# Optimization experiments

Hardware: AMD Instinct MI355X
Metric: run time of the kernel (lower is better)

The kernel has to match this reference:

```python
import jax, jax.numpy as jnp
import numpy as np

E = 8          # num_experts
TOP_K = 2      # router top-k
ALPHA = 1.702  # swigluoai alpha
LIMIT = 7.0    # swigluoai clamp limit


def setup_inputs() -> dict:
    key = jax.random.key(0)
    ks = jax.random.split(key, 7)
    B, S, H, I = 2, 1024, 1024, 1024
    s = 1.0 / np.sqrt(H)  # keep activations O(1), realistic init scale
    return {
        "x": jax.random.normal(ks[0], (B, S, H), jnp.float32),
        "router_weight": jax.random.normal(ks[1], (E, H), jnp.float32) * s,
        "router_bias": jax.random.normal(ks[2], (E,), jnp.float32) * 0.01,
        "w1": jax.random.normal(ks[3], (E, H, 2 * I), jnp.float32) * s,  # interleaved gate/up
        "w1_bias": jax.random.normal(ks[4], (E, 2 * I), jnp.float32) * 0.01,
        "w2": jax.random.normal(ks[5], (E, I, H), jnp.float32) * s,
        "w2_bias": jax.random.normal(ks[6], (E, H), jnp.float32) * 0.01,
    }


def _moe(x, router_weight, router_bias, w1, w1_bias, w2, w2_bias):
    B, S, H = x.shape
    xf = x.reshape(-1, H)                                   # [T, H]
    # ---- router: softmax over expert logits, then top-k ----
    logits = xf @ router_weight.T + router_bias             # [T, E]
    probs = jax.nn.softmax(logits, axis=-1)
    expert_weights, expert_ids = jax.lax.top_k(probs, TOP_K)  # [T, k]
    # combine weights scattered to dense [T, E] (no normalization: normalize_expert_weights=None)
    combine = jnp.sum(jax.nn.one_hot(expert_ids, E, dtype=xf.dtype)
                      * expert_weights[..., None], axis=1)  # [T, E]
    # ---- grouped MLP, expressed densely per expert (reference semantics) ----
    h = jnp.einsum('th,ehi->eti', xf, w1) + w1_bias[:, None, :]   # [E, T, 2I]
    gate = h[..., 0::2]                                          # interleaved layout
    up = h[..., 1::2]
    gate = jnp.minimum(gate, LIMIT)                              # swigluoai: clamp gate max
    up = jnp.clip(up, -LIMIT, LIMIT)                             # clamp up both sides
    glu = gate * jax.nn.sigmoid(gate * ALPHA)
    act = (up + 1.0) * glu                                       # [E, T, I]
    y = jnp.einsum('eti,eih->eth', act, w2) + w2_bias[:, None, :]  # [E, T, H]
    out = jnp.einsum('eth,te->th', y, combine)                   # weighted combine
    return out.reshape(B, S, H), expert_weights


def reference(x, router_weight, router_bias, w1, w1_bias, w2, w2_bias):
    return _moe(x, router_weight, router_bias, w1, w1_bias, w2, w2_bias)
```

## Files before the change

kernel.cpp:

```cpp
#include <hip/hip_runtime.h>
#include <cstdint>
#include <cstddef>

typedef unsigned short u16;
typedef unsigned int u32;
typedef short bf16x8 __attribute__((ext_vector_type(8)));
typedef float floatx4 __attribute__((ext_vector_type(4)));

#define GLD16(gp, sp) __builtin_amdgcn_global_load_lds(                      \
    (const __attribute__((address_space(1))) void*)(gp),                     \
    (__attribute__((address_space(3))) void*)(sp), 16, 0, 0)

__device__ __forceinline__ u16 f2bf(float f) {
  unsigned u = __float_as_uint(f);
  u += 0x7fffu + ((u >> 16) & 1u);
  return (u16)(u >> 16);
}

__global__ __launch_bounds__(256) void prep_kernel(
    const float* __restrict__ x, const float* __restrict__ rw, const float* __restrict__ rbias,
    u16* __restrict__ xb, float* __restrict__ ew,
    int* __restrict__ row_token, float* __restrict__ row_scale, int* __restrict__ cnt) {
  const int b = blockIdx.x, tid = threadIdx.x;
  if (b < 1024) {
    const float4* in4 = (const float4*)x;
    ushort4* out4 = (ushort4*)xb;
    int i = (b << 8) + tid;
#pragma unroll
    for (int rep = 0; rep < 2; ++rep, i += 262144) {
      float4 v = in4[i];
      ushort4 o;
      o.x = f2bf(v.x); o.y = f2bf(v.y); o.z = f2bf(v.z); o.w = f2bf(v.w);
      out4[i] = o;
    }
  } else {
    const int wave = tid >> 6, lane = tid & 63;
    const int t = ((b - 1024) << 2) + wave;
    const float4* xv = (const float4*)(x + (size_t)t * 1024);
    float acc[8];
#pragma unroll
    for (int e = 0; e < 8; ++e) acc[e] = 0.f;
    for (int j = lane; j < 256; j += 64) {
      float4 xx = xv[j];
#pragma unroll
      for (int e = 0; e < 8; ++e) {
        float4 wv = ((const float4*)(rw + (size_t)e * 1024))[j];
        acc[e] += xx.x * wv.x + xx.y * wv.y + xx.z * wv.z + xx.w * wv.w;
      }
    }
#pragma unroll
    for (int e = 0; e < 8; ++e) {
      float v = acc[e];
#pragma unroll
      for (int off = 32; off > 0; off >>= 1) v += __shfl_down(v, off);
      acc[e] = v;
    }
    if (lane == 0) {
      float p[8];
      float mx = -1e30f;
#pragma unroll
      for (int e = 0; e < 8; ++e) { p[e] = acc[e] + rbias[e]; mx = fmaxf(mx, p[e]); }
      float sum = 0.f;
#pragma unroll
      for (int e = 0; e < 8; ++e) { p[e] = __expf(p[e] - mx); sum += p[e]; }
      float inv = 1.f / sum;
#pragma unroll
      for (int e = 0; e < 8; ++e) p[e] *= inv;
      int i0 = 0;
#pragma unroll
      for (int e = 1; e < 8; ++e) if (p[e] > p[i0]) i0 = e;
      int i1 = (i0 == 0) ? 1 : 0;
#pragma unroll
      for (int e = 0; e < 8; ++e) if (e != i0 && e != i1 && p[e] > p[i1]) i1 = e;
      ew[t * 2 + 0] = p[i0];
      ew[t * 2 + 1] = p[i1];
      int s0 = atomicAdd(&cnt[i0], 1);
      row_token[(i0 << 11) + s0] = t;
      row_scale[(i0 << 11) + s0] = p[i0];
      int s1 = atomicAdd(&cnt[i1], 1);
      row_token[(i1 << 11) + s1] = t;
      row_scale[(i1 << 11) + s1] = p[i1];
    }
  }
}

__device__ __forceinline__ void stage_bt(const float* __restrict__ src0, int C, int idx,
                                         u16* __restrict__ Bs) {
  const int n = idx & 127, q = idx >> 7;
  const float* src = src0 + (size_t)(q * 8) * C + n;
  float f[8];
#pragma unroll
  for (int j = 0; j < 8; ++j) f[j] = src[(size_t)j * C];
  u32 pk[4];
#pragma unroll
  for (int m = 0; m < 4; ++m) pk[m] = (u32)f2bf(f[2 * m]) | ((u32)f2bf(f[2 * m + 1]) << 16);
  *(uint4*)(Bs + ((n >> 4) << 9) + (q << 7) + ((n & 15) << 3)) =
      make_uint4(pk[0], pk[1], pk[2], pk[3]);
}

__global__ __launch_bounds__(256) void gemm1_act_kernel(
    const u16* __restrict__ xb, const float* __restrict__ w1,
    const float* __restrict__ w1b,
    const int* __restrict__ row_token, const float* __restrict__ row_scale,
    const int* __restrict__ cnt, u16* __restrict__ actS) {
  const int d = blockIdx.x;
  const int xcd = d & 7, j = d >> 3;
  const int colHi = j & 1, rb = (j >> 1) & 15, e = j >> 5;
  if (rb * 128 >= cnt[e]) return;
  const int colBase = (xcd + (colHi << 3)) << 7;
  const int slotB = (e << 11) + (rb << 7);
  __shared__ __align__(16) u16 As[4096];
  __shared__ __align__(16) u16 Bs[4096];
  const int tid = threadIdx.x, lane = tid & 63, wave = tid >> 6;
  const int row16 = lane & 15, chunk = lane >> 4;
  const float* w1e = w1 + (size_t)e * 2097152 + colBase;
  int tk0 = row_token[slotB + wave * 16 + row16];       if (tk0 < 0) tk0 = 0;
  int tk1 = row_token[slotB + (wave + 4) * 16 + row16]; if (tk1 < 0) tk1 = 0;
  const u16* aP0 = xb + (size_t)tk0 * 1024 + chunk * 8;
  const u16* aP1 = xb + (size_t)tk1 * 1024 + chunk * 8;
  const int wr = wave >> 1, wc = wave & 1;
  floatx4 acc[4][4];
#pragma unroll
  for (int mi = 0; mi < 4; ++mi)
#pragma unroll
    for (int ni = 0; ni < 4; ++ni) acc[mi][ni] = floatx4{0.f, 0.f, 0.f, 0.f};

  for (int kt = 0; kt < 32; ++kt) {
    const int k = kt * 32;
    GLD16(aP0 + k, As + wave * 512);
    GLD16(aP1 + k, As + (wave + 4) * 512);
    stage_bt(w1e + (size_t)k * 2048, 2048, tid, Bs);
    stage_bt(w1e + (size_t)k * 2048, 2048, tid + 256, Bs);
    __syncthreads();
    bf16x8 af[4], bfr[4];
#pragma unroll
    for (int mi = 0; mi < 4; ++mi) af[mi] = *(const bf16x8*)(As + (wr * 4 + mi) * 512 + lane * 8);
#pragma unroll
    for (int ni = 0; ni < 4; ++ni) bfr[ni] = *(const bf16x8*)(Bs + (wc * 4 + ni) * 512 + lane * 8);
#pragma unroll
    for (int mi = 0; mi < 4; ++mi)
#pragma unroll
      for (int ni = 0; ni < 4; ++ni)
        acc[mi][ni] = __builtin_amdgcn_mfma_f32_16x16x32_bf16(af[mi], bfr[ni], acc[mi][ni], 0, 0, 0);
    __syncthreads();
  }

  const int cl = lane & 15, ql = lane >> 4;
#pragma unroll
  for (int mi = 0; mi < 4; ++mi) {
#pragma unroll
    for (int r = 0; r < 4; ++r) {
      const int slot = slotB + wr * 64 + mi * 16 + ql * 4 + r;
      const float c = row_scale[slot];
#pragma unroll
      for (int ni = 0; ni < 4; ++ni) {
        const int n = colBase + wc * 64 + ni * 16 + cl;
        float v = acc[mi][ni][r] + w1b[e * 2048 + n];
        float o = __shfl_xor(v, 1);
        if ((lane & 1) == 0) {
          float g = fminf(v, 7.f);
          float u = fminf(fmaxf(o, -7.f), 7.f);
          float sg = 1.f / (1.f + __expf(-1.702f * g));
          float a = (u + 1.f) * (g * sg);
          actS[(size_t)slot * 1024 + (n >> 1)] = f2bf(c * a);
        }
      }
    }
  }
}

__global__ __launch_bounds__(256) void gemm2_add_kernel(
    const u16* __restrict__ actS, const float* __restrict__ w2, const float* __restrict__ w2b,
    const int* __restrict__ row_token, const float* __restrict__ row_scale,
    const int* __restrict__ cnt, float* __restrict__ out) {
  const int d = blockIdx.x;
  const int xcd = d & 7, j = d >> 3;
  const int ks = j & 1, rb = (j >> 1) & 15, e = j >> 5;
  if (rb * 128 >= cnt[e]) return;
  const int colBase = xcd << 7;
  const int slotB = (e << 11) + (rb << 7);
  const int k0 = ks << 9;
  __shared__ __align__(16) u16 As[4096];
  __shared__ __align__(16) u16 Bs[4096];
  const int tid = threadIdx.x, lane = tid & 63, wave = tid >> 6;
  const int row16 = lane & 15, chunk = lane >> 4;
  const float* w2e = w2 + (size_t)e * 1048576 + (size_t)k0 * 1024 + colBase;
  const u16* aP0 = actS + (size_t)(slotB + wave * 16 + row16) * 1024 + k0 + chunk * 8;
  const u16* aP1 = actS + (size_t)(slotB + (wave + 4) * 16 + row16) * 1024 + k0 + chunk * 8;
  const int wr = wave >> 1, wc = wave & 1;
  floatx4 acc[4][4];
#pragma unroll
  for (int mi = 0; mi < 4; ++mi)
#pragma unroll
    for (int ni = 0; ni < 4; ++ni) acc[mi][ni] = floatx4{0.f, 0.f, 0.f, 0.f};

  for (int kt = 0; kt < 16; ++kt) {
    const int k = kt * 32;
    GLD16(aP0 + k, As + wave * 512);
    GLD16(aP1 + k, As + (wave + 4) * 512);
    stage_bt(w2e + (size_t)k * 1024, 1024, tid, Bs);
    stage_bt(w2e + (size_t)k * 1024, 1024, tid + 256, Bs);
    __syncthreads();
    bf16x8 af[4], bfr[4];
#pragma unroll
    for (int mi = 0; mi < 4; ++mi) af[mi] = *(const bf16x8*)(As + (wr * 4 + mi) * 512 + lane * 8);
#pragma unroll
    for (int ni = 0; ni < 4; ++ni) bfr[ni] = *(const bf16x8*)(Bs + (wc * 4 + ni) * 512 + lane * 8);
#pragma unroll
    for (int mi = 0; mi < 4; ++mi)
#pragma unroll
      for (int ni = 0; ni < 4; ++ni)
        acc[mi][ni] = __builtin_amdgcn_mfma_f32_16x16x32_bf16(af[mi], bfr[ni], acc[mi][ni], 0, 0, 0);
    __syncthreads();
  }

  const int cl = lane & 15, ql = lane >> 4;
#pragma unroll
  for (int mi = 0; mi < 4; ++mi)
#pragma unroll
    for (int r = 0; r < 4; ++r) {
      const int slot = slotB + wr * 64 + mi * 16 + ql * 4 + r;
      const int tok = row_token[slot];
      if (tok < 0) continue;
      const float p = row_scale[slot];
#pragma unroll
      for (int ni = 0; ni < 4; ++ni) {
        const int col = colBase + wc * 64 + ni * 16 + cl;
        float v = acc[mi][ni][r];
        if (ks == 0) v += p * w2b[e * 1024 + col];
        atomicAdd(out + (size_t)tok * 1024 + col, v);
      }
    }
}

extern "C" void kernel_launch(void* const* d_in, const int* in_sizes, int n_in,
                              void* d_out, int out_size, void* d_ws, size_t ws_size,
                              hipStream_t stream) {
  const float* x   = (const float*)d_in[0];
  const float* rw  = (const float*)d_in[1];
  const float* rb  = (const float*)d_in[2];
  const float* w1  = (const float*)d_in[3];
  const float* w1b = (const float*)d_in[4];
  const float* w2  = (const float*)d_in[5];
  const float* w2b = (const float*)d_in[6];
  float* out = (float*)d_out;
  float* ew  = out + (size_t)2048 * 1024;

  char* ws = (char*)d_ws;
  u16* xb          = (u16*)(ws);
  u16* actS        = (u16*)(ws + (4ull << 20));
  int* row_token   = (int*)(ws + (36ull << 20));
  float* row_scale = (float*)(ws + (36ull << 20) + (64 << 10));
  int* cnt         = (int*)(ws + (36ull << 20) + (128 << 10));

  hipMemsetAsync(out, 0, (size_t)2048 * 1024 * 4, stream);
  hipMemsetAsync(row_token, 0xFF, 64 << 10, stream);
  hipMemsetAsync(row_scale, 0, (64 << 10) + 32, stream);
  prep_kernel<<<1536, 256, 0, stream>>>(x, rw, rb, xb, ew, row_token, row_scale, cnt);
  gemm1_act_kernel<<<2048, 256, 0, stream>>>(xb, w1, w1b, row_token, row_scale, cnt, actS);
  gemm2_add_kernel<<<2048, 256, 0, stream>>>(actS, w2, w2b, row_token, row_scale, cnt, out);
}
```

Measured before the change: 303.9 us.

## Double-buffer LDS tiles and prefetch next K-slice in both expert GEMMs

Both grouped GEMM kernels now keep two LDS buffers for A and B. The next K-slice of fp32 weights is loaded into registers and the next A tile is issued via global_load_lds before the MFMAs on the current buffer run. The weights are converted to bf16 and written to the other buffer after compute, which cuts the barriers per iteration from two to one. This is meant to hide global load latency behind compute, at the cost of double the LDS and 16 extra registers per thread.

```diff
diff --git a/kernel.cpp b/kernel.cpp
--- a/kernel.cpp
+++ b/kernel.cpp
@@ -84,13 +84,16 @@
   }
 }
 
-__device__ __forceinline__ void stage_bt(const float* __restrict__ src0, int C, int idx,
+__device__ __forceinline__ void load_b8(const float* __restrict__ src0, int C, int idx,
+                                        float* __restrict__ f) {
+  const int n = idx & 127, q = idx >> 7;
+  const float* src = src0 + (size_t)(q * 8) * C + n;
+#pragma unroll
+  for (int j = 0; j < 8; ++j) f[j] = src[(size_t)j * C];
+}
+__device__ __forceinline__ void write_b8(const float* __restrict__ f, int idx,
                                          u16* __restrict__ Bs) {
   const int n = idx & 127, q = idx >> 7;
-  const float* src = src0 + (size_t)(q * 8) * C + n;
-  float f[8];
-#pragma unroll
-  for (int j = 0; j < 8; ++j) f[j] = src[(size_t)j * C];
   u32 pk[4];
 #pragma unroll
   for (int m = 0; m < 4; ++m) pk[m] = (u32)f2bf(f[2 * m]) | ((u32)f2bf(f[2 * m + 1]) << 16);
@@ -109,8 +112,8 @@
   if (rb * 128 >= cnt[e]) return;
   const int colBase = (xcd + (colHi << 3)) << 7;
   const int slotB = (e << 11) + (rb << 7);
-  __shared__ __align__(16) u16 As[4096];
-  __shared__ __align__(16) u16 Bs[4096];
+  __shared__ __align__(16) u16 As[2][4096];
+  __shared__ __align__(16) u16 Bs[2][4096];
   const int tid = threadIdx.x, lane = tid & 63, wave = tid >> 6;
   const int row16 = lane & 15, chunk = lane >> 4;
   const float* w1e = w1 + (size_t)e * 2097152 + colBase;
@@ -125,24 +128,41 @@
 #pragma unroll
     for (int ni = 0; ni < 4; ++ni) acc[mi][ni] = floatx4{0.f, 0.f, 0.f, 0.f};
 
+  float fb[16];
+  load_b8(w1e, 2048, tid, fb);
+  load_b8(w1e, 2048, tid + 256, fb + 8);
+  write_b8(fb, tid, Bs[0]);
+  write_b8(fb + 8, tid + 256, Bs[0]);
+  GLD16(aP0, As[0] + wave * 512);
+  GLD16(aP1, As[0] + (wave + 4) * 512);
+
   for (int kt = 0; kt < 32; ++kt) {
-    const int k = kt * 32;
-    GLD16(aP0 + k, As + wave * 512);
-    GLD16(aP1 + k, As + (wave + 4) * 512);
-    stage_bt(w1e + (size_t)k * 2048, 2048, tid, Bs);
-    stage_bt(w1e + (size_t)k * 2048, 2048, tid + 256, Bs);
+    const int p = kt & 1;
     __syncthreads();
+    if (kt < 31) {
+      const float* wsrc = w1e + (size_t)(kt + 1) * 32 * 2048;
+      load_b8(wsrc, 2048, tid, fb);
+      load_b8(wsrc, 2048, tid + 256, fb + 8);
+      const int k = (kt + 1) * 32;
+      GLD16(aP0 + k, As[1 - p] + wave * 512);
+      GLD16(aP1 + k, As[1 - p] + (wave + 4) * 512);
+    }
     bf16x8 af[4], bfr[4];
 #pragma unroll
-    for (int mi = 0; mi < 4; ++mi) af[mi] = *(const bf16x8*)(As + (wr * 4 + mi) * 512 + lane * 8);
-#pragma unroll
-    for (int ni = 0; ni < 4; ++ni) bfr[ni] = *(const bf16x8*)(Bs + (wc * 4 + ni) * 512 + lane * 8);
+    for (int mi = 0; mi < 4; ++mi)
+      af[mi] = *(const bf16x8*)(As[p] + (wr * 4 + mi) * 512 + lane * 8);
+#pragma unroll
+    for (int ni = 0; ni < 4; ++ni)
+      bfr[ni] = *(const bf16x8*)(Bs[p] + (wc * 4 + ni) * 512 + lane * 8);
 #pragma unroll
     for (int mi = 0; mi < 4; ++mi)
 #pragma unroll
       for (int ni = 0; ni < 4; ++ni)
         acc[mi][ni] = __builtin_amdgcn_mfma_f32_16x16x32_bf16(af[mi], bfr[ni], acc[mi][ni], 0, 0, 0);
-    __syncthreads();
+    if (kt < 31) {
+      write_b8(fb, tid, Bs[1 - p]);
+      write_b8(fb + 8, tid + 256, Bs[1 - p]);
+    }
   }
 
   const int cl = lane & 15, ql = lane >> 4;
@@ -180,8 +200,8 @@
   const int colBase = xcd << 7;
   const int slotB = (e << 11) + (rb << 7);
   const int k0 = ks << 9;
-  __shared__ __align__(16) u16 As[4096];
-  __shared__ __align__(16) u16 Bs[4096];
+  __shared__ __align__(16) u16 As[2][4096];
+  __shared__ __align__(16) u16 Bs[2][4096];
   const int tid = threadIdx.x, lane = tid & 63, wave = tid >> 6;
   const int row16 = lane & 15, chunk = lane >> 4;
   const float* w2e = w2 + (size_t)e * 1048576 + (size_t)k0 * 1024 + colBase;
@@ -194,24 +214,41 @@
 #pragma unroll
     for (int ni = 0; ni < 4; ++ni) acc[mi][ni] = floatx4{0.f, 0.f, 0.f, 0.f};
 
+  float fb[16];
+  load_b8(w2e, 1024, tid, fb);
+  load_b8(w2e, 1024, tid + 256, fb + 8);
+  write_b8(fb, tid, Bs[0]);
+  write_b8(fb + 8, tid + 256, Bs[0]);
+  GLD16(aP0, As[0] + wave * 512);
+  GLD16(aP1, As[0] + (wave + 4) * 512);
+
   for (int kt = 0; kt < 16; ++kt) {
-    const int k = kt * 32;
-    GLD16(aP0 + k, As + wave * 512);
-    GLD16(aP1 + k, As + (wave + 4) * 512);
-    stage_bt(w2e + (size_t)k * 1024, 1024, tid, Bs);
-    stage_bt(w2e + (size_t)k * 1024, 1024, tid + 256, Bs);
+    const int p = kt & 1;
     __syncthreads();
+    if (kt < 15) {
+      const float* wsrc = w2e + (size_t)(kt + 1) * 32 * 1024;
+      load_b8(wsrc, 1024, tid, fb);
+      load_b8(wsrc, 1024, tid + 256, fb + 8);
+      const int k = (kt + 1) * 32;
+      GLD16(aP0 + k, As[1 - p] + wave * 512);
+      GLD16(aP1 + k, As[1 - p] + (wave + 4) * 512);
+    }
     bf16x8 af[4], bfr[4];
 #pragma unroll
-    for (int mi = 0; mi < 4; ++mi) af[mi] = *(const bf16x8*)(As + (wr * 4 + mi) * 512 + lane * 8);
-#pragma unroll
-    for (int ni = 0; ni < 4; ++ni) bfr[ni] = *(const bf16x8*)(Bs + (wc * 4 + ni) * 512 + lane * 8);
+    for (int mi = 0; mi < 4; ++mi)
+      af[mi] = *(const bf16x8*)(As[p] + (wr * 4 + mi) * 512 + lane * 8);
+#pragma unroll
+    for (int ni = 0; ni < 4; ++ni)
+      bfr[ni] = *(const bf16x8*)(Bs[p] + (wc * 4 + ni) * 512 + lane * 8);
 #pragma unroll
     for (int mi = 0; mi < 4; ++mi)
 #pragma unroll
       for (int ni = 0; ni < 4; ++ni)
         acc[mi][ni] = __builtin_amdgcn_mfma_f32_16x16x32_bf16(af[mi], bfr[ni], acc[mi][ni], 0, 0, 0);
-    __syncthreads();
+    if (kt < 15) {
+      write_b8(fb, tid, Bs[1 - p]);
+      write_b8(fb + 8, tid + 256, Bs[1 - p]);
+    }
   }
 
   const int cl = lane & 15, ql = lane >> 4;
```

New measurement: 305.0 us. About the same (+0.4%).
